# Kernel optimization log

Measured on AMD Instinct MI355X. Metric: run time of the kernel, lower is better.

The kernel has to match this reference:

```python
import jax, jax.numpy as jnp
import numpy as np

EPS = 1e-08

def _compute_W(V, C, eps=EPS):
    # W = H_k ... H_1, applied sequentially as in the torch loop
    W = jnp.eye(C, dtype=V.dtype)
    def step(W, v):
        v = v / (jnp.linalg.norm(v) + eps)
        # H @ W = W - 2 v (v^T W)
        W = W - 2.0 * jnp.outer(v, v @ W)
        return W, None
    W, _ = jax.lax.scan(step, W, V)
    return W

def setup_inputs() -> dict:
    key = jax.random.key(0)
    k1, k2 = jax.random.split(key)
    x = jax.random.normal(k1, (16, 512, 64, 64), dtype=jnp.float32)
    V = jax.random.normal(k2, (32, 512), dtype=jnp.float32)
    return {"x": x, "V": V}

def reference(x, V):
    B, C, H, Wd = x.shape
    W = _compute_W(V, C)  # [C, C] orthogonal
    # 1x1 conv: out[b,o,h,w] = sum_c W[o,c] * x[b,c,h,w]
    return jnp.einsum('oc,bchw->bohw', W, x)
```

## Files before the change

### kernel.cpp

```cpp
#include <hip/hip_runtime.h>
#include <hip/hip_bf16.h>
#include <stdint.h>
#include <stddef.h>

#define HH_EPS 1e-8f

typedef __attribute__((ext_vector_type(8))) short short8;
typedef __attribute__((ext_vector_type(4))) float f32x4;

__global__ void compute_w(const float* __restrict__ V,
                          __hip_bfloat16* __restrict__ Wb) {
    const int wave = threadIdx.x >> 6;
    const int lane = threadIdx.x & 63;
    const int jA = (blockIdx.x * 4 + wave) * 2;
    const int jB = jA + 1;
    const int ib = lane * 8;

    float wA[8], wB[8];
    #pragma unroll
    for (int r = 0; r < 8; r++) {
        wA[r] = (ib + r == jA) ? 1.0f : 0.0f;
        wB[r] = (ib + r == jB) ? 1.0f : 0.0f;
    }

    float4 c0 = *(const float4*)(V + ib);
    float4 c1 = *(const float4*)(V + ib + 4);

    for (int k = 0; k < 32; k++) {
        const float v[8] = {c0.x, c0.y, c0.z, c0.w, c1.x, c1.y, c1.z, c1.w};
        if (k < 31) {
            c0 = *(const float4*)(V + (size_t)(k + 1) * 512 + ib);
            c1 = *(const float4*)(V + (size_t)(k + 1) * 512 + ib + 4);
        }
        float dA = 0.0f, dB = 0.0f, ss = 0.0f;
        #pragma unroll
        for (int r = 0; r < 8; r++) {
            dA += v[r] * wA[r];
            dB += v[r] * wB[r];
            ss += v[r] * v[r];
        }
        #pragma unroll
        for (int off = 32; off > 0; off >>= 1) {
            dA += __shfl_xor(dA, off);
            dB += __shfl_xor(dB, off);
            ss += __shfl_xor(ss, off);
        }
        const float t = sqrtf(ss) + HH_EPS;
        const float scale = 2.0f / (t * t);
        const float tA = scale * dA, tB = scale * dB;
        #pragma unroll
        for (int r = 0; r < 8; r++) {
            wA[r] -= tA * v[r];
            wB[r] -= tB * v[r];
        }
    }
    #pragma unroll
    for (int r = 0; r < 8; r++) {
        Wb[(size_t)(ib + r) * 512 + jA] = __float2bfloat16(wA[r]);
        Wb[(size_t)(ib + r) * 512 + jB] = __float2bfloat16(wB[r]);
    }
}

#define BM 128
#define BN 128
#define BK 32
#define CDIM 512
#define SDIM 4096
#define BROW 40

__device__ __forceinline__ void issue_loads(
    const float* __restrict__ xb, const __hip_bfloat16* __restrict__ Wb,
    int k0, int m0, int n0, int tid, short8 a_pf[2], float b_pf[16])
{
    #pragma unroll
    for (int c = 0; c < 2; c++) {
        const int chunk = c * 256 + tid;
        const int row = chunk >> 2, seg = chunk & 3;
        a_pf[c] = *(const short8*)(Wb + (size_t)(m0 + row) * CDIM + k0 + seg * 8);
    }
    #pragma unroll
    for (int c = 0; c < 2; c++) {
        const int u = c * 256 + tid;
        const int n = u & 127, kg = u >> 7;
        const float* gp = xb + (size_t)(k0 + kg * 8) * SDIM + n0 + n;
        #pragma unroll
        for (int j = 0; j < 8; j++) b_pf[c * 8 + j] = gp[(size_t)j * SDIM];
    }
}

__device__ __forceinline__ void write_lds(
    __hip_bfloat16* __restrict__ Al, __hip_bfloat16* __restrict__ Bl,
    int tid, const short8 a_pf[2], const float b_pf[16])
{
    #pragma unroll
    for (int c = 0; c < 2; c++) {
        const int chunk = c * 256 + tid;
        *(short8*)(&Al[chunk * 8]) = a_pf[c];
    }
    #pragma unroll
    for (int c = 0; c < 2; c++) {
        const int u = c * 256 + tid;
        const int n = u & 127, kg = u >> 7;
        short8 pk;
        #pragma unroll
        for (int j = 0; j < 8; j++) {
            __hip_bfloat16 h = __float2bfloat16(b_pf[c * 8 + j]);
            pk[j] = *(short*)&h;
        }
        *(short8*)(&Bl[n * BROW + kg * 8]) = pk;
    }
}

__global__ __launch_bounds__(256, 3) void hh_gemm(
    const float* __restrict__ x,
    const __hip_bfloat16* __restrict__ Wb,
    float* __restrict__ out)
{
    __shared__ __attribute__((aligned(16))) __hip_bfloat16 Alds[2][BM * BK];
    __shared__ __attribute__((aligned(16))) __hip_bfloat16 Blds[2][BN * BROW];

    const int tid  = threadIdx.x;
    const int wave = tid >> 6, lane = tid & 63;
    const int quad = lane >> 4, l16 = lane & 15;
    const int wm = wave >> 1, wn = wave & 1;

    const int bid  = blockIdx.x;
    const int mt   = bid >> 9;
    const int rest = bid & 511;
    const int b    = rest >> 5;
    const int nt   = rest & 31;
    const int m0 = mt * BM, n0 = nt * BN;

    const float* xb = x + (size_t)b * CDIM * SDIM;

    f32x4 acc[4][4];
    #pragma unroll
    for (int i = 0; i < 4; i++)
        #pragma unroll
        for (int jj = 0; jj < 4; jj++) {
            f32x4 z = {0.0f, 0.0f, 0.0f, 0.0f};
            acc[i][jj] = z;
        }

    short8 a_pf[2];
    float  b_pf[16];

    issue_loads(xb, Wb, 0, m0, n0, tid, a_pf, b_pf);
    write_lds(Alds[0], Blds[0], tid, a_pf, b_pf);
    __syncthreads();

    for (int kt = 0; kt < CDIM / BK; kt++) {
        const int cur = kt & 1;

        if (kt < CDIM / BK - 1)
            issue_loads(xb, Wb, (kt + 1) * BK, m0, n0, tid, a_pf, b_pf);

        short8 af[4], bfr[4];
        #pragma unroll
        for (int mi = 0; mi < 4; mi++)
            af[mi] = *(const short8*)(&Alds[cur][(wm * 64 + mi * 16 + l16) * BK + quad * 8]);
        #pragma unroll
        for (int ni = 0; ni < 4; ni++)
            bfr[ni] = *(const short8*)(&Blds[cur][(wn * 64 + ni * 16 + l16) * BROW + quad * 8]);
        #pragma unroll
        for (int mi = 0; mi < 4; mi++)
            #pragma unroll
            for (int ni = 0; ni < 4; ni++)
                acc[mi][ni] = __builtin_amdgcn_mfma_f32_16x16x32_bf16(
                    af[mi], bfr[ni], acc[mi][ni], 0, 0, 0);

        if (kt < CDIM / BK - 1)
            write_lds(Alds[cur ^ 1], Blds[cur ^ 1], tid, a_pf, b_pf);
        __syncthreads();
    }

    float* ob = out + (size_t)b * CDIM * SDIM;
    #pragma unroll
    for (int mi = 0; mi < 4; mi++) {
        #pragma unroll
        for (int ni = 0; ni < 4; ni++) {
            const int col = n0 + wn * 64 + ni * 16 + l16;
            #pragma unroll
            for (int r = 0; r < 4; r++) {
                const int row = m0 + wm * 64 + mi * 16 + quad * 4 + r;
                ob[(size_t)row * SDIM + col] = acc[mi][ni][r];
            }
        }
    }
}

extern "C" void kernel_launch(void* const* d_in, const int* in_sizes, int n_in,
                              void* d_out, int out_size, void* d_ws, size_t ws_size,
                              hipStream_t stream) {
    const float* x = (const float*)d_in[0];
    const float* V = (const float*)d_in[1];
    float* out = (float*)d_out;

    __hip_bfloat16* Wb = (__hip_bfloat16*)d_ws;

    compute_w<<<64, 256, 0, stream>>>(V, Wb);
    hh_gemm<<<2048, 256, 0, stream>>>(x, Wb, out);
}
```

Measured before the change: 299.1 us.

## Cover all output channels per block and stream pre-swizzled W fragments from global

Each block now computes all 512 output channels for a 64-wide spatial tile, so each x element is read from HBM once instead of four times. W is written by compute_w in an MFMA-fragment-swizzled layout and loaded straight into registers, which removes the A LDS tile. B loads are prefetched two steps ahead and a custom waitcnt+barrier replaces __syncthreads. The 8x4 accumulator array raises register pressure (launch bounds 2) and the grid halves to 1024 blocks.

```diff
diff --git a/kernel.cpp b/kernel.cpp
--- a/kernel.cpp
+++ b/kernel.cpp
@@ -8,8 +8,20 @@
 typedef __attribute__((ext_vector_type(8))) short short8;
 typedef __attribute__((ext_vector_type(4))) float f32x4;
 
+#define CDIM 512
+#define SDIM 4096
+#define BN 64
+#define BK 32
+#define NSTEP 16
+#define BROW 40
+
+__device__ __forceinline__ size_t wt_idx(int o, int c) {
+    return ((size_t)((c >> 5) * 32 + (o >> 4)) * 64
+            + (size_t)((o & 15) * 4 + ((c >> 3) & 3))) * 8 + (c & 7);
+}
+
 __global__ void compute_w(const float* __restrict__ V,
-                          __hip_bfloat16* __restrict__ Wb) {
+                          __hip_bfloat16* __restrict__ Wt) {
     const int wave = threadIdx.x >> 6;
     const int lane = threadIdx.x & 63;
     const int jA = (blockIdx.x * 4 + wave) * 2;
@@ -56,133 +68,113 @@
     }
     #pragma unroll
     for (int r = 0; r < 8; r++) {
-        Wb[(size_t)(ib + r) * 512 + jA] = __float2bfloat16(wA[r]);
-        Wb[(size_t)(ib + r) * 512 + jB] = __float2bfloat16(wB[r]);
+        Wt[wt_idx(ib + r, jA)] = __float2bfloat16(wA[r]);
+        Wt[wt_idx(ib + r, jB)] = __float2bfloat16(wB[r]);
     }
 }
 
-#define BM 128
-#define BN 128
-#define BK 32
-#define CDIM 512
-#define SDIM 4096
-#define BROW 40
-
-__device__ __forceinline__ void issue_loads(
-    const float* __restrict__ xb, const __hip_bfloat16* __restrict__ Wb,
-    int k0, int m0, int n0, int tid, short8 a_pf[2], float b_pf[16])
-{
-    #pragma unroll
-    for (int c = 0; c < 2; c++) {
-        const int chunk = c * 256 + tid;
-        const int row = chunk >> 2, seg = chunk & 3;
-        a_pf[c] = *(const short8*)(Wb + (size_t)(m0 + row) * CDIM + k0 + seg * 8);
-    }
-    #pragma unroll
-    for (int c = 0; c < 2; c++) {
-        const int u = c * 256 + tid;
-        const int n = u & 127, kg = u >> 7;
-        const float* gp = xb + (size_t)(k0 + kg * 8) * SDIM + n0 + n;
-        #pragma unroll
-        for (int j = 0; j < 8; j++) b_pf[c * 8 + j] = gp[(size_t)j * SDIM];
-    }
+__device__ __forceinline__ void lds_barrier() {
+    asm volatile("" ::: "memory");
+    __builtin_amdgcn_s_waitcnt(0xC07F);
+    __builtin_amdgcn_s_barrier();
+    asm volatile("" ::: "memory");
 }
 
-__device__ __forceinline__ void write_lds(
-    __hip_bfloat16* __restrict__ Al, __hip_bfloat16* __restrict__ Bl,
-    int tid, const short8 a_pf[2], const float b_pf[16])
-{
-    #pragma unroll
-    for (int c = 0; c < 2; c++) {
-        const int chunk = c * 256 + tid;
-        *(short8*)(&Al[chunk * 8]) = a_pf[c];
-    }
-    #pragma unroll
-    for (int c = 0; c < 2; c++) {
-        const int u = c * 256 + tid;
-        const int n = u & 127, kg = u >> 7;
-        short8 pk;
-        #pragma unroll
-        for (int j = 0; j < 8; j++) {
-            __hip_bfloat16 h = __float2bfloat16(b_pf[c * 8 + j]);
-            pk[j] = *(short*)&h;
-        }
-        *(short8*)(&Bl[n * BROW + kg * 8]) = pk;
-    }
-}
-
-__global__ __launch_bounds__(256, 3) void hh_gemm(
+__global__ __launch_bounds__(256, 2) void hh_gemm(
     const float* __restrict__ x,
-    const __hip_bfloat16* __restrict__ Wb,
+    const short8* __restrict__ Wt16,
     float* __restrict__ out)
 {
-    __shared__ __attribute__((aligned(16))) __hip_bfloat16 Alds[2][BM * BK];
     __shared__ __attribute__((aligned(16))) __hip_bfloat16 Blds[2][BN * BROW];
 
     const int tid  = threadIdx.x;
     const int wave = tid >> 6, lane = tid & 63;
     const int quad = lane >> 4, l16 = lane & 15;
-    const int wm = wave >> 1, wn = wave & 1;
 
-    const int bid  = blockIdx.x;
-    const int mt   = bid >> 9;
-    const int rest = bid & 511;
-    const int b    = rest >> 5;
-    const int nt   = rest & 31;
-    const int m0 = mt * BM, n0 = nt * BN;
+    const int bid = blockIdx.x;
+    const int b   = bid >> 6;
+    const int nt  = bid & 63;
+    const int n0  = nt * BN;
 
     const float* xb = x + (size_t)b * CDIM * SDIM;
 
-    f32x4 acc[4][4];
+    const int bn = tid & 63, kg = tid >> 6;
+    const float* xp0 = xb + (size_t)(kg * 8) * SDIM + n0 + bn;
+
+    f32x4 acc[8][4];
     #pragma unroll
-    for (int i = 0; i < 4; i++)
+    for (int mi = 0; mi < 8; mi++)
         #pragma unroll
-        for (int jj = 0; jj < 4; jj++) {
+        for (int ni = 0; ni < 4; ni++) {
             f32x4 z = {0.0f, 0.0f, 0.0f, 0.0f};
-            acc[i][jj] = z;
+            acc[mi][ni] = z;
         }
 
-    short8 a_pf[2];
-    float  b_pf[16];
+    short8 af[2][8];
+    float  pfB[2][8];
 
-    issue_loads(xb, Wb, 0, m0, n0, tid, a_pf, b_pf);
-    write_lds(Alds[0], Blds[0], tid, a_pf, b_pf);
-    __syncthreads();
+    auto loadB = [&](int kt, float* dst) {
+        const float* p = xp0 + (size_t)kt * BK * SDIM;
+        #pragma unroll
+        for (int j = 0; j < 8; j++) dst[j] = p[(size_t)j * SDIM];
+    };
+    auto writeB = [&](int buf, const float* src) {
+        short8 pk;
+        #pragma unroll
+        for (int j = 0; j < 8; j++) {
+            __hip_bfloat16 h = __float2bfloat16(src[j]);
+            pk[j] = *(short*)&h;
+        }
+        *(short8*)(&Blds[buf][bn * BROW + kg * 8]) = pk;
+    };
+    auto loadA = [&](int kt, short8* dst) {
+        const short8* p = Wt16 + (size_t)kt * 2048 + (size_t)(wave * 8) * 64
+                        + l16 * 4 + quad;
+        #pragma unroll
+        for (int mi = 0; mi < 8; mi++) dst[mi] = p[mi * 64];
+    };
 
-    for (int kt = 0; kt < CDIM / BK; kt++) {
-        const int cur = kt & 1;
+    loadB(0, pfB[0]);
+    loadB(1, pfB[1]);
+    loadA(0, af[0]);
+    writeB(0, pfB[0]);
+    lds_barrier();
 
-        if (kt < CDIM / BK - 1)
-            issue_loads(xb, Wb, (kt + 1) * BK, m0, n0, tid, a_pf, b_pf);
-
-        short8 af[4], bfr[4];
-        #pragma unroll
-        for (int mi = 0; mi < 4; mi++)
-            af[mi] = *(const short8*)(&Alds[cur][(wm * 64 + mi * 16 + l16) * BK + quad * 8]);
+    auto step = [&](int kt, int p, bool pfb, bool pfa, bool last) {
+        if (pfb) loadB(kt + 2, pfB[p]);
+        if (pfa) loadA(kt + 1, af[p ^ 1]);
+        short8 bfr[4];
         #pragma unroll
         for (int ni = 0; ni < 4; ni++)
-            bfr[ni] = *(const short8*)(&Blds[cur][(wn * 64 + ni * 16 + l16) * BROW + quad * 8]);
+            bfr[ni] = *(const short8*)(&Blds[p][(ni * 16 + l16) * BROW + quad * 8]);
         #pragma unroll
-        for (int mi = 0; mi < 4; mi++)
+        for (int mi = 0; mi < 8; mi++)
             #pragma unroll
             for (int ni = 0; ni < 4; ni++)
                 acc[mi][ni] = __builtin_amdgcn_mfma_f32_16x16x32_bf16(
-                    af[mi], bfr[ni], acc[mi][ni], 0, 0, 0);
+                    af[p][mi], bfr[ni], acc[mi][ni], 0, 0, 0);
+        if (!last) {
+            writeB(p ^ 1, pfB[p ^ 1]);
+            lds_barrier();
+        }
+    };
 
-        if (kt < CDIM / BK - 1)
-            write_lds(Alds[cur ^ 1], Blds[cur ^ 1], tid, a_pf, b_pf);
-        __syncthreads();
+    for (int kt = 0; kt < NSTEP - 2; kt += 2) {
+        step(kt,     0, true, true, false);
+        step(kt + 1, 1, true, true, false);
     }
+    step(NSTEP - 2, 0, false, true,  false);
+    step(NSTEP - 1, 1, false, false, true);
 
-    float* ob = out + (size_t)b * CDIM * SDIM;
+    float* ob = out + (size_t)b * CDIM * SDIM + n0;
     #pragma unroll
-    for (int mi = 0; mi < 4; mi++) {
+    for (int mi = 0; mi < 8; mi++) {
         #pragma unroll
         for (int ni = 0; ni < 4; ni++) {
-            const int col = n0 + wn * 64 + ni * 16 + l16;
+            const int col = ni * 16 + l16;
             #pragma unroll
             for (int r = 0; r < 4; r++) {
-                const int row = m0 + wm * 64 + mi * 16 + quad * 4 + r;
+                const int row = wave * 128 + mi * 16 + quad * 4 + r;
                 ob[(size_t)row * SDIM + col] = acc[mi][ni][r];
             }
         }
@@ -196,8 +188,8 @@
     const float* V = (const float*)d_in[1];
     float* out = (float*)d_out;
 
-    __hip_bfloat16* Wb = (__hip_bfloat16*)d_ws;
+    __hip_bfloat16* Wt = (__hip_bfloat16*)d_ws;
 
-    compute_w<<<64, 256, 0, stream>>>(V, Wb);
-    hh_gemm<<<2048, 256, 0, stream>>>(x, Wb, out);
+    compute_w<<<64, 256, 0, stream>>>(V, Wt);
+    hh_gemm<<<1024, 256, 0, stream>>>(x, (const short8*)Wt, out);
 }
```

Result: faster. 284.0 us (-5.0%).
